# Performance work log

Hardware: AMD Instinct MI355X
Metric: run time of the kernel (lower is better)

Reference implementation:

```python
import jax, jax.numpy as jnp
import numpy as np

EMBED = 1024
HEADS = 16
HEAD_DIM = EMBED // HEADS


def setup_inputs() -> dict:
    key = jax.random.key(0)
    ks = jax.random.split(key, 11)
    B, L, D = 2, 2048, EMBED
    s = 0.02
    return {
        "q": jax.random.normal(ks[0], (B, L, D), jnp.float32),
        "k": jax.random.normal(ks[1], (B, L, D), jnp.float32),
        "v": jax.random.normal(ks[2], (B, L, D), jnp.float32),
        "w_q": jax.random.normal(ks[3], (D, D), jnp.float32) * s,
        "b_q": jnp.zeros((D,), jnp.float32),
        "w_k": jax.random.normal(ks[4], (D, D), jnp.float32) * s,
        "b_k": jnp.zeros((D,), jnp.float32),
        "w_v": jax.random.normal(ks[5], (D, D), jnp.float32) * s,
        "b_v": jnp.zeros((D,), jnp.float32),
        "w_o": jax.random.normal(ks[6], (D, D), jnp.float32) * s,
        "b_o": jnp.zeros((D,), jnp.float32),
    }


def reference(q, k, v, w_q, b_q, w_k, b_k, w_v, b_v, w_o, b_o):
    B, L, D = q.shape
    H, Dh = HEADS, HEAD_DIM
    # Linear projections (torch Linear: x @ W.T + b)
    qp = (q @ w_q.T + b_q).reshape(B, L, H, Dh)
    kp = (k @ w_k.T + b_k).reshape(B, L, H, Dh)
    vp = (v @ w_v.T + b_v).reshape(B, L, H, Dh)
    # energy: [n, h, q, k]
    energy = jnp.einsum("nqhd,nkhd->nhqk", qp, kp)
    scale = 1.0 / jnp.sqrt(jnp.asarray(Dh, qp.dtype))
    attn = jax.nn.softmax(energy * scale, axis=-1)
    ctx = jnp.einsum("nhql,nlhd->nqhd", attn, vp).reshape(B, L, D)
    return ctx @ w_o.T + b_o
```

## Files before the change

### kernel.cpp

```cpp
#include <hip/hip_runtime.h>

typedef __bf16 bf16;
typedef __bf16 bf16x2 __attribute__((ext_vector_type(2)));
typedef __bf16 bf16x4 __attribute__((ext_vector_type(4)));
typedef __bf16 bf16x8 __attribute__((ext_vector_type(8)));
typedef float f32x4 __attribute__((ext_vector_type(4)));

#define MFMA16(a, b, c) __builtin_amdgcn_mfma_f32_16x16x32_bf16((a), (b), (c), 0, 0, 0)

#define QSCALE 0.18033688011112042f

__device__ inline void gld16(const void* g, void* l) {
    __builtin_amdgcn_global_load_lds(
        (const __attribute__((address_space(1))) unsigned int*)g,
        (__attribute__((address_space(3))) unsigned int*)l, 16, 0, 0);
}

__device__ inline bf16x8 cvt8(float4 a, float4 b) {
    bf16x8 v;
    v[0] = (bf16)a.x; v[1] = (bf16)a.y; v[2] = (bf16)a.z; v[3] = (bf16)a.w;
    v[4] = (bf16)b.x; v[5] = (bf16)b.y; v[6] = (bf16)b.z; v[7] = (bf16)b.w;
    return v;
}

__global__ __launch_bounds__(256) void cvt7_kernel(
    const float* __restrict__ q,  bf16* __restrict__ qb,
    const float* __restrict__ k,  bf16* __restrict__ kb,
    const float* __restrict__ v,  bf16* __restrict__ vb,
    const float* __restrict__ wq, bf16* __restrict__ wqb,
    const float* __restrict__ wk, bf16* __restrict__ wkb,
    const float* __restrict__ wv, bf16* __restrict__ wvb,
    const float* __restrict__ wo, bf16* __restrict__ wob)
{
    const float* src; bf16* dst; int n;
    switch (blockIdx.y) {
        case 0: src = q;  dst = qb;  n = 1 << 22; break;
        case 1: src = k;  dst = kb;  n = 1 << 22; break;
        case 2: src = v;  dst = vb;  n = 1 << 22; break;
        case 3: src = wq; dst = wqb; n = 1 << 20; break;
        case 4: src = wk; dst = wkb; n = 1 << 20; break;
        case 5: src = wv; dst = wvb; n = 1 << 20; break;
        default: src = wo; dst = wob; n = 1 << 20; break;
    }
    int i = (blockIdx.x * 256 + threadIdx.x) * 8;
    if (i < n) {
        float4 a = *(const float4*)&src[i];
        float4 b = *(const float4*)&src[i + 4];
        *(bf16x8*)&dst[i] = cvt8(a, b);
    }
}

__global__ __launch_bounds__(256) void cvt3_kernel(
    const float* __restrict__ s0, bf16* __restrict__ d0,
    const float* __restrict__ s1, bf16* __restrict__ d1,
    const float* __restrict__ s2, bf16* __restrict__ d2)
{
    const float* src = blockIdx.y == 0 ? s0 : blockIdx.y == 1 ? s1 : s2;
    bf16*        dst = blockIdx.y == 0 ? d0 : blockIdx.y == 1 ? d1 : d2;
    int i = (blockIdx.x * 256 + threadIdx.x) * 8;
    float4 a = *(const float4*)&src[i];
    float4 b = *(const float4*)&src[i + 4];
    *(bf16x8*)&dst[i] = cvt8(a, b);
}

__global__ __launch_bounds__(256) void cvt_kernel(
    const float* __restrict__ src, bf16* __restrict__ dst, int n)
{
    int i = (blockIdx.x * 256 + threadIdx.x) * 8;
    if (i < n) {
        float4 a = *(const float4*)&src[i];
        float4 b = *(const float4*)&src[i + 4];
        *(bf16x8*)&dst[i] = cvt8(a, b);
    }
}

__global__ __launch_bounds__(256) void qkv_bf16(
    const bf16* __restrict__ qb, const bf16* __restrict__ kb,
    const bf16* __restrict__ vb,
    const bf16* __restrict__ wq, const float* __restrict__ bq,
    const bf16* __restrict__ wk, const float* __restrict__ bk,
    const bf16* __restrict__ wv, const float* __restrict__ bv,
    bf16* __restrict__ Qp, bf16* __restrict__ Kp, bf16* __restrict__ Vt)
{
    __shared__ __align__(16) bf16 sm[16896];
    bf16* As = sm;
    bf16* Bs = sm + 8192;
    bf16* Ts = sm;

    const int id  = blockIdx.x;
    const int pr  = (id >> 6) * 8 + (id & 7);
    const int proj = pr >> 5;
    const int m0  = (pr & 31) * 128;
    const int n0  = ((id >> 3) & 7) * 128;

    const bf16*  A    = proj == 0 ? qb : proj == 1 ? kb : vb;
    const bf16*  B    = proj == 0 ? wq : proj == 1 ? wk : wv;
    const float* bias = proj == 0 ? bq : proj == 1 ? bk : bv;

    const int tid  = threadIdx.x;
    const int lane = tid & 63;
    const int w    = tid >> 6;
    const int g    = lane >> 4;
    const int ln   = lane & 15;
    const int rowb = (w & 1) * 64;
    const int colb = (w >> 1) * 64;
    const int ro   = lane >> 3, lc = lane & 7;

    auto issue = [&](int t) {
        int k0 = t * 64;
        for (int j = 0; j < 4; ++j) {
            int base = w * 32 + j * 8;
            int row  = base + ro;
            int c    = lc ^ (row & 7);
            gld16(&A[(size_t)(m0 + row) * 1024 + k0 + c * 8], &As[base * 64]);
            gld16(&B[(size_t)(n0 + row) * 1024 + k0 + c * 8], &Bs[base * 64]);
        }
    };

    issue(0);
    f32x4 acc[4][4] = {};

    for (int t = 0; t < 16; ++t) {
        __syncthreads();
        for (int ks = 0; ks < 2; ++ks) {
            bf16x8 af[4], bfm[4];
            for (int mi = 0; mi < 4; ++mi) {
                int row = rowb + mi * 16 + ln;
                af[mi] = *(const bf16x8*)&As[row * 64 + ((ks * 4 + g) ^ (ln & 7)) * 8];
            }
            for (int ni = 0; ni < 4; ++ni) {
                int row = colb + ni * 16 + ln;
                bfm[ni] = *(const bf16x8*)&Bs[row * 64 + ((ks * 4 + g) ^ (ln & 7)) * 8];
            }
            for (int mi = 0; mi < 4; ++mi)
                for (int ni = 0; ni < 4; ++ni)
                    acc[mi][ni] = MFMA16(af[mi], bfm[ni], acc[mi][ni]);
        }
        __syncthreads();
        if (t < 15) issue(t + 1);
    }

    if (proj != 2) {
        for (int mi = 0; mi < 4; ++mi) {
            for (int ni = 0; ni < 4; ++ni) {
                int col = n0 + colb + ni * 16 + ln;
                float bv_ = bias[col];
                int rowbase = m0 + rowb + mi * 16 + g * 4;
                if (proj == 0) {
                    for (int r = 0; r < 4; ++r)
                        Qp[(size_t)(rowbase + r) * 1024 + col] =
                            (bf16)((acc[mi][ni][r] + bv_) * QSCALE);
                } else {
                    for (int r = 0; r < 4; ++r)
                        Kp[(size_t)(rowbase + r) * 1024 + col] =
                            (bf16)(acc[mi][ni][r] + bv_);
                }
            }
        }
    } else {
        for (int mi = 0; mi < 4; ++mi) {
            for (int ni = 0; ni < 4; ++ni) {
                int col = colb + ni * 16 + ln;
                float bv_ = bias[n0 + col];
                int row = rowb + mi * 16 + g * 4;
                bf16x4 pk;
                for (int r = 0; r < 4; ++r) pk[r] = (bf16)(acc[mi][ni][r] + bv_);
                *(bf16x4*)&Ts[col * 132 + row] = pk;
            }
        }
        __syncthreads();
        const int bidx = m0 >> 11;
        const int tok0 = m0 & 2047;
        for (int i = 0; i < 8; ++i) {
            int c    = tid + 256 * i;
            int col  = c >> 4;
            int t64  = (c >> 3) & 1;
            int cc   = c & 7;
            int gcol = n0 + col;
            union { bf16 e[8]; uint4 u; } tmp;
            for (int j = 0; j < 8; ++j) {
                int s = 2 * cc + (j >> 2) + ((j & 3) << 4);
                tmp.e[j] = Ts[col * 132 + t64 * 64 + s];
            }
            size_t dst = ((size_t)(bidx * 16 + (gcol >> 6)) * 64 + (gcol & 63)) * 2048
                         + tok0 + t64 * 64 + cc * 8;
            *(uint4*)&Vt[dst] = tmp.u;
        }
    }
}

__global__ __launch_bounds__(256) void qkv_gemm(
    const float* __restrict__ q, const float* __restrict__ k,
    const float* __restrict__ v,
    const bf16* __restrict__ wq, const float* __restrict__ bq,
    const bf16* __restrict__ wk, const float* __restrict__ bk,
    const bf16* __restrict__ wv, const float* __restrict__ bv,
    bf16* __restrict__ Qp, bf16* __restrict__ Kp, bf16* __restrict__ Vt)
{
    __shared__ __align__(16) bf16 sm[8192 + 2 * 8192];
    bf16* As = sm;
    bf16* Bs = sm + 8192;
    bf16* Ts = sm;

    const int id  = blockIdx.x;
    const int pr  = (id >> 6) * 8 + (id & 7);
    const int proj = pr >> 5;
    const int m0  = (pr & 31) * 128;
    const int n0  = ((id >> 3) & 7) * 128;

    const float* A    = proj == 0 ? q  : proj == 1 ? k  : v;
    const bf16*  B    = proj == 0 ? wq : proj == 1 ? wk : wv;
    const float* bias = proj == 0 ? bq : proj == 1 ? bk : bv;

    const int tid  = threadIdx.x;
    const int lane = tid & 63;
    const int w    = tid >> 6;
    const int g    = lane >> 4;
    const int ln   = lane & 15;
    const int rowb = (w & 1) * 64;
    const int colb = (w >> 1) * 64;
    const int srow = tid >> 3, slc = tid & 7;
    const int ro   = lane >> 3, lc = lane & 7;

    float4 ra[4][2];
    for (int i = 0; i < 4; ++i) {
        const float* p = &A[(size_t)(m0 + srow + 32 * i) * 1024 + slc * 8];
        ra[i][0] = *(const float4*)p;
        ra[i][1] = *(const float4*)(p + 4);
    }
    for (int j = 0; j < 4; ++j) {
        int base = w * 32 + j * 8;
        int row  = base + ro;
        int c    = lc ^ (row & 7);
        gld16(&B[(size_t)(n0 + row) * 1024 + c * 8], &Bs[base * 64]);
    }

    f32x4 acc[4][4] = {};

    for (int t = 0; t < 16; ++t) {
        __syncthreads();
        for (int i = 0; i < 4; ++i) {
            int row = srow + 32 * i;
            *(bf16x8*)&As[row * 64 + (slc ^ (row & 7)) * 8] = cvt8(ra[i][0], ra[i][1]);
        }
        __syncthreads();
        if (t < 15) {
            int k1 = (t + 1) * 64;
            for (int i = 0; i < 4; ++i) {
                const float* p = &A[(size_t)(m0 + srow + 32 * i) * 1024 + k1 + slc * 8];
                ra[i][0] = *(const float4*)p;
                ra[i][1] = *(const float4*)(p + 4);
            }
            int bsel = (t + 1) & 1;
            for (int j = 0; j < 4; ++j) {
                int base = w * 32 + j * 8;
                int row  = base + ro;
                int c    = lc ^ (row & 7);
                gld16(&B[(size_t)(n0 + row) * 1024 + k1 + c * 8],
                      &Bs[bsel * 8192 + base * 64]);
            }
        }
        const bf16* Bt = Bs + (t & 1) * 8192;
        for (int ks = 0; ks < 2; ++ks) {
            bf16x8 af[4], bfm[4];
            for (int mi = 0; mi < 4; ++mi) {
                int row = rowb + mi * 16 + ln;
                af[mi] = *(const bf16x8*)&As[row * 64 + ((ks * 4 + g) ^ (ln & 7)) * 8];
            }
            for (int ni = 0; ni < 4; ++ni) {
                int row = colb + ni * 16 + ln;
                bfm[ni] = *(const bf16x8*)&Bt[row * 64 + ((ks * 4 + g) ^ (ln & 7)) * 8];
            }
            for (int mi = 0; mi < 4; ++mi)
                for (int ni = 0; ni < 4; ++ni)
                    acc[mi][ni] = MFMA16(af[mi], bfm[ni], acc[mi][ni]);
        }
    }

    if (proj != 2) {
        for (int mi = 0; mi < 4; ++mi) {
            for (int ni = 0; ni < 4; ++ni) {
                int col = n0 + colb + ni * 16 + ln;
                float bv_ = bias[col];
                int rowbase = m0 + rowb + mi * 16 + g * 4;
                if (proj == 0) {
                    for (int r = 0; r < 4; ++r)
                        Qp[(size_t)(rowbase + r) * 1024 + col] =
                            (bf16)((acc[mi][ni][r] + bv_) * QSCALE);
                } else {
                    for (int r = 0; r < 4; ++r)
                        Kp[(size_t)(rowbase + r) * 1024 + col] =
                            (bf16)(acc[mi][ni][r] + bv_);
                }
            }
        }
    } else {
        __syncthreads();
        for (int mi = 0; mi < 4; ++mi) {
            for (int ni = 0; ni < 4; ++ni) {
                int col = colb + ni * 16 + ln;
                float bv_ = bias[n0 + col];
                int row = rowb + mi * 16 + g * 4;
                bf16x4 pk;
                for (int r = 0; r < 4; ++r) pk[r] = (bf16)(acc[mi][ni][r] + bv_);
                *(bf16x4*)&Ts[col * 132 + row] = pk;
            }
        }
        __syncthreads();
        const int bidx = m0 >> 11;
        const int tok0 = m0 & 2047;
        for (int i = 0; i < 8; ++i) {
            int c    = tid + 256 * i;
            int col  = c >> 4;
            int t64  = (c >> 3) & 1;
            int cc   = c & 7;
            int gcol = n0 + col;
            union { bf16 e[8]; uint4 u; } tmp;
            for (int j = 0; j < 8; ++j) {
                int s = 2 * cc + (j >> 2) + ((j & 3) << 4);
                tmp.e[j] = Ts[col * 132 + t64 * 64 + s];
            }
            size_t dst = ((size_t)(bidx * 16 + (gcol >> 6)) * 64 + (gcol & 63)) * 2048
                         + tok0 + t64 * 64 + cc * 8;
            *(uint4*)&Vt[dst] = tmp.u;
        }
    }
}

__global__ __launch_bounds__(256) void gemm_out(
    const bf16* __restrict__ A, const bf16* __restrict__ B,
    const float* __restrict__ bias, float* __restrict__ C)
{
    __shared__ __align__(16) bf16 sm[2 * 4096 + 2 * 8192];
    bf16* As = sm;
    bf16* Bs = sm + 8192;

    const int id = blockIdx.x;
    const int m0 = ((id >> 6) * 8 + (id & 7)) * 64;
    const int n0 = ((id >> 3) & 7) * 128;

    const int tid  = threadIdx.x;
    const int lane = tid & 63;
    const int w    = tid >> 6;
    const int g    = lane >> 4;
    const int ln   = lane & 15;
    const int rowb = (w & 1) * 32;
    const int colb = (w >> 1) * 64;
    const int ro   = lane >> 3, lc = lane & 7;

    auto issue = [&](int t) {
        int k0 = t * 64, sel = t & 1;
        for (int j = 0; j < 2; ++j) {
            int base = w * 16 + j * 8;
            int row  = base + ro;
            int c    = lc ^ (row & 7);
            gld16(&A[(size_t)(m0 + row) * 1024 + k0 + c * 8],
                  &As[sel * 4096 + base * 64]);
        }
        for (int j = 0; j < 4; ++j) {
            int base = w * 32 + j * 8;
            int row  = base + ro;
            int c    = lc ^ (row & 7);
            gld16(&B[(size_t)(n0 + row) * 1024 + k0 + c * 8],
                  &Bs[sel * 8192 + base * 64]);
        }
    };

    issue(0);
    f32x4 acc[2][4] = {};

    for (int t = 0; t < 16; ++t) {
        __syncthreads();
        if (t < 15) issue(t + 1);
        const bf16* At = As + (t & 1) * 4096;
        const bf16* Bt = Bs + (t & 1) * 8192;
        for (int ks = 0; ks < 2; ++ks) {
            bf16x8 af[2], bfm[4];
            for (int mi = 0; mi < 2; ++mi) {
                int row = rowb + mi * 16 + ln;
                af[mi] = *(const bf16x8*)&At[row * 64 + ((ks * 4 + g) ^ (ln & 7)) * 8];
            }
            for (int ni = 0; ni < 4; ++ni) {
                int row = colb + ni * 16 + ln;
                bfm[ni] = *(const bf16x8*)&Bt[row * 64 + ((ks * 4 + g) ^ (ln & 7)) * 8];
            }
            for (int mi = 0; mi < 2; ++mi)
                for (int ni = 0; ni < 4; ++ni)
                    acc[mi][ni] = MFMA16(af[mi], bfm[ni], acc[mi][ni]);
        }
    }

    for (int mi = 0; mi < 2; ++mi) {
        for (int ni = 0; ni < 4; ++ni) {
            int col = n0 + colb + ni * 16 + ln;
            float bv_ = bias[col];
            int rowbase = m0 + rowb + mi * 16 + g * 4;
            for (int r = 0; r < 4; ++r)
                C[(size_t)(rowbase + r) * 1024 + col] = acc[mi][ni][r] + bv_;
        }
    }
}

__global__ __launch_bounds__(256, 2) void attn_kernel(
    const bf16* __restrict__ Qp, const bf16* __restrict__ Kp,
    const bf16* __restrict__ Vt, bf16* __restrict__ Ctx)
{
    __shared__ __align__(16) bf16 smem[2 * 4096 + 2 * 4096];
    bf16* Ks = smem;
    bf16* Vs = smem + 8192;

    const int id = blockIdx.x;
    const int qt = (id >> 3) & 15;
    const int bh = (id & 7) + ((id >> 7) << 3);

    const int tid  = threadIdx.x;
    const int lane = tid & 63;
    const int w    = tid >> 6;
    const int g    = lane >> 4;
    const int ln   = lane & 15;
    const int ro   = lane >> 3, lc = lane & 7;
    const size_t rowQ0 = (size_t)(bh >> 4) * 2048 + qt * 128;
    const size_t rowK0 = (size_t)(bh >> 4) * 2048;
    const int hcol = (bh & 15) * 64;
    const bf16* VtB = Vt + (size_t)bh * 64 * 2048;

    for (int j = 0; j < 2; ++j) {
        int base = w * 16 + j * 8;
        int row  = base + ro;
        int c    = lc ^ (row & 7);
        gld16(&Kp[(rowK0 + row) * 1024 + hcol + c * 8], &Ks[base * 64]);
        gld16(&VtB[(size_t)row * 2048 + c * 8], &Vs[base * 64]);
    }

    bf16x8 qf[2][2];
#pragma unroll
    for (int u = 0; u < 2; ++u)
#pragma unroll
        for (int ks = 0; ks < 2; ++ks)
            qf[u][ks] = *(const bf16x8*)&Qp[(rowQ0 + w * 32 + u * 16 + ln) * 1024
                                            + hcol + ks * 32 + g * 8];

    bf16x8 ones;
#pragma unroll
    for (int i = 0; i < 8; ++i) ones[i] = (bf16)1.0f;

    f32x4 oacc[2][4] = {};
    f32x4 lacc[2] = {};

    __syncthreads();

    for (int t = 0; t < 32; ++t) {
        if (t < 31) {
            int sel = (t + 1) & 1, kvo = (t + 1) * 64;
            for (int j = 0; j < 2; ++j) {
                int base = w * 16 + j * 8;
                int kv   = base + ro;
                int c    = lc ^ (kv & 7);
                gld16(&Kp[(rowK0 + kvo + kv) * 1024 + hcol + c * 8],
                      &Ks[sel * 4096 + base * 64]);
                gld16(&VtB[(size_t)kv * 2048 + kvo + c * 8],
                      &Vs[sel * 4096 + base * 64]);
            }
        }
        const bf16* Kt  = Ks + (t & 1) * 4096;
        const bf16* Vti = Vs + (t & 1) * 4096;

        f32x4 sf[2][4] = {};
#pragma unroll
        for (int ks = 0; ks < 2; ++ks) {
            bf16x8 kf[4];
#pragma unroll
            for (int nj = 0; nj < 4; ++nj) {
                int row = nj * 16 + ln;
                kf[nj] = *(const bf16x8*)&Kt[row * 64 + ((ks * 4 + g) ^ (ln & 7)) * 8];
            }
            __builtin_amdgcn_s_setprio(1);
#pragma unroll
            for (int u = 0; u < 2; ++u)
#pragma unroll
                for (int nj = 0; nj < 4; ++nj)
                    sf[u][nj] = MFMA16(kf[nj], qf[u][ks], sf[u][nj]);
            __builtin_amdgcn_s_setprio(0);
        }

        unsigned W[2][4][2];
#pragma unroll
        for (int u = 0; u < 2; ++u)
#pragma unroll
            for (int r = 0; r < 4; ++r)
#pragma unroll
                for (int h = 0; h < 2; ++h) {
                    bf16x2 t2;
                    t2[0] = (bf16)__builtin_amdgcn_exp2f(sf[u][2 * h][r]);
                    t2[1] = (bf16)__builtin_amdgcn_exp2f(sf[u][2 * h + 1][r]);
                    W[u][r][h] = __builtin_bit_cast(unsigned, t2);
                }
#pragma unroll
        for (int u = 0; u < 2; ++u)
#pragma unroll
            for (int h = 0; h < 2; ++h) {
                asm("v_permlane16_swap_b32 %0, %1" : "+v"(W[u][0][h]), "+v"(W[u][2][h]));
                asm("v_permlane32_swap_b32 %0, %1" : "+v"(W[u][0][h]), "+v"(W[u][2][h]));
                asm("v_permlane16_swap_b32 %0, %1" : "+v"(W[u][1][h]), "+v"(W[u][3][h]));
                asm("v_permlane32_swap_b32 %0, %1" : "+v"(W[u][1][h]), "+v"(W[u][3][h]));
            }

#pragma unroll
        for (int ks = 0; ks < 2; ++ks) {
            bf16x8 vf[4];
#pragma unroll
            for (int nd = 0; nd < 4; ++nd) {
                int row = nd * 16 + ln;
                vf[nd] = *(const bf16x8*)&Vti[row * 64 + ((ks * 4 + g) ^ (ln & 7)) * 8];
            }
            __builtin_amdgcn_s_setprio(1);
#pragma unroll
            for (int u = 0; u < 2; ++u) {
                union { unsigned uw[4]; bf16x8 v; } pf;
                pf.uw[0] = W[u][2 * ks][0];     pf.uw[1] = W[u][2 * ks][1];
                pf.uw[2] = W[u][2 * ks + 1][0]; pf.uw[3] = W[u][2 * ks + 1][1];
                lacc[u] = MFMA16(pf.v, ones, lacc[u]);
#pragma unroll
                for (int nd = 0; nd < 4; ++nd)
                    oacc[u][nd] = MFMA16(pf.v, vf[nd], oacc[u][nd]);
            }
            __builtin_amdgcn_s_setprio(0);
        }
        __syncthreads();
    }

#pragma unroll
    for (int u = 0; u < 2; ++u)
#pragma unroll
        for (int r = 0; r < 4; ++r) {
            float inv = 1.0f / lacc[u][r];
            size_t row = rowQ0 + w * 32 + u * 16 + g * 4 + r;
#pragma unroll
            for (int nd = 0; nd < 4; ++nd)
                Ctx[row * 1024 + hcol + nd * 16 + ln] = (bf16)(oacc[u][nd][r] * inv);
        }
}

extern "C" void kernel_launch(void* const* d_in, const int* in_sizes, int n_in,
                              void* d_out, int out_size, void* d_ws, size_t ws_size,
                              hipStream_t stream)
{
    const float* q  = (const float*)d_in[0];
    const float* k  = (const float*)d_in[1];
    const float* v  = (const float*)d_in[2];
    const float* wq = (const float*)d_in[3];
    const float* bq = (const float*)d_in[4];
    const float* wk = (const float*)d_in[5];
    const float* bk = (const float*)d_in[6];
    const float* wv = (const float*)d_in[7];
    const float* bv = (const float*)d_in[8];
    const float* wo = (const float*)d_in[9];
    const float* bo = (const float*)d_in[10];
    float* out = (float*)d_out;

    const int D = 1024;
    bf16* W  = (bf16*)d_ws;
    bf16* Qp = W;
    bf16* Kp = W + (1u << 22);
    bf16* Vt = W + (2u << 22);
    bf16* Ctx = Qp;

    if (ws_size >= (size_t)40 * 1024 * 1024) {
        bf16* vb  = W + (3u << 22);
        bf16* wqb = W + (1u << 24);
        bf16* wkb = wqb + (1u << 20);
        bf16* wvb = wkb + (1u << 20);
        bf16* wob = wvb + (1u << 20);
        bf16* qb  = (bf16*)d_out;
        bf16* kb  = qb + (1u << 22);

        cvt7_kernel<<<dim3(2048, 7), 256, 0, stream>>>(
            q, qb, k, kb, v, vb, wq, wqb, wk, wkb, wv, wvb, wo, wob);
        qkv_bf16<<<768, 256, 0, stream>>>(qb, kb, vb, wqb, bq, wkb, bk, wvb, bv,
                                          Qp, Kp, Vt);
        attn_kernel<<<512, 256, 0, stream>>>(Qp, Kp, Vt, Ctx);
        gemm_out<<<512, 256, 0, stream>>>(Ctx, wob, bo, out);
    } else {
        bf16* wqb = (bf16*)d_out;
        bf16* wkb = wqb + (size_t)D * D;
        bf16* wvb = wkb + (size_t)D * D;
        bf16* wob = Kp;

        cvt3_kernel<<<dim3(512, 3), 256, 0, stream>>>(wq, wqb, wk, wkb, wv, wvb);
        qkv_gemm<<<768, 256, 0, stream>>>(q, k, v, wqb, bq, wkb, bk, wvb, bv,
                                          Qp, Kp, Vt);
        attn_kernel<<<512, 256, 0, stream>>>(Qp, Kp, Vt, Ctx);
        cvt_kernel<<<512, 256, 0, stream>>>(wo, wob, D * D);
        gemm_out<<<512, 256, 0, stream>>>(Ctx, wob, bo, out);
    }
}
```

Before: 208.4 us.

## Split attention KV range across two wave groups and merge partials in LDS

The attention block grows to 512 threads: two groups of four waves each process half of the key/value sequence for the same 128 query rows, each with its own double-buffered LDS tiles. At the end, group 0 writes its unnormalized output and row sums to shared memory, and group 1 adds them to its own before normalizing and storing. This shortens the serial KV loop per wave and raises waves per CU to hide latency. It costs more LDS per block (64KB), an extra reduction step and barrier, and occupancy limits from the larger shared memory footprint. The merge needs no max rescaling because the kernel already skips the running max in its softmax.

```diff
diff --git a/kernel.cpp b/kernel.cpp
--- a/kernel.cpp
+++ b/kernel.cpp
@@ -401,13 +401,15 @@
     }
 }
 
-__global__ __launch_bounds__(256, 2) void attn_kernel(
+__global__ __launch_bounds__(512, 4) void attn_kernel(
     const bf16* __restrict__ Qp, const bf16* __restrict__ Kp,
     const bf16* __restrict__ Vt, bf16* __restrict__ Ctx)
 {
-    __shared__ __align__(16) bf16 smem[2 * 4096 + 2 * 4096];
+    __shared__ __align__(16) bf16 smem[32768];
     bf16* Ks = smem;
-    bf16* Vs = smem + 8192;
+    bf16* Vs = smem + 16384;
+    float* O_sh = (float*)smem;
+    float* l_sh = (float*)smem + 64 * 132;
 
     const int id = blockIdx.x;
     const int qt = (id >> 3) & 15;
@@ -416,20 +418,25 @@
     const int tid  = threadIdx.x;
     const int lane = tid & 63;
     const int w    = tid >> 6;
+    const int h    = w >> 2;
+    const int wl   = w & 3;
     const int g    = lane >> 4;
     const int ln   = lane & 15;
     const int ro   = lane >> 3, lc = lane & 7;
+    const int kvb  = h * 1024;
     const size_t rowQ0 = (size_t)(bh >> 4) * 2048 + qt * 128;
     const size_t rowK0 = (size_t)(bh >> 4) * 2048;
     const int hcol = (bh & 15) * 64;
     const bf16* VtB = Vt + (size_t)bh * 64 * 2048;
 
     for (int j = 0; j < 2; ++j) {
-        int base = w * 16 + j * 8;
+        int base = wl * 16 + j * 8;
         int row  = base + ro;
         int c    = lc ^ (row & 7);
-        gld16(&Kp[(rowK0 + row) * 1024 + hcol + c * 8], &Ks[base * 64]);
-        gld16(&VtB[(size_t)row * 2048 + c * 8], &Vs[base * 64]);
+        gld16(&Kp[(rowK0 + kvb + row) * 1024 + hcol + c * 8],
+              &Ks[(h * 2 + 0) * 4096 + base * 64]);
+        gld16(&VtB[(size_t)row * 2048 + kvb + c * 8],
+              &Vs[(h * 2 + 0) * 4096 + base * 64]);
     }
 
     bf16x8 qf[2][2];
@@ -437,7 +444,7 @@
     for (int u = 0; u < 2; ++u)
 #pragma unroll
         for (int ks = 0; ks < 2; ++ks)
-            qf[u][ks] = *(const bf16x8*)&Qp[(rowQ0 + w * 32 + u * 16 + ln) * 1024
+            qf[u][ks] = *(const bf16x8*)&Qp[(rowQ0 + wl * 32 + u * 16 + ln) * 1024
                                             + hcol + ks * 32 + g * 8];
 
     bf16x8 ones;
@@ -449,21 +456,21 @@
 
     __syncthreads();
 
-    for (int t = 0; t < 32; ++t) {
-        if (t < 31) {
-            int sel = (t + 1) & 1, kvo = (t + 1) * 64;
+    for (int t = 0; t < 16; ++t) {
+        if (t < 15) {
+            int sel = (t + 1) & 1, kvo = kvb + (t + 1) * 64;
             for (int j = 0; j < 2; ++j) {
-                int base = w * 16 + j * 8;
-                int kv   = base + ro;
-                int c    = lc ^ (kv & 7);
-                gld16(&Kp[(rowK0 + kvo + kv) * 1024 + hcol + c * 8],
-                      &Ks[sel * 4096 + base * 64]);
-                gld16(&VtB[(size_t)kv * 2048 + kvo + c * 8],
-                      &Vs[sel * 4096 + base * 64]);
-            }
-        }
-        const bf16* Kt  = Ks + (t & 1) * 4096;
-        const bf16* Vti = Vs + (t & 1) * 4096;
+                int base = wl * 16 + j * 8;
+                int row  = base + ro;
+                int c    = lc ^ (row & 7);
+                gld16(&Kp[(rowK0 + kvo + row) * 1024 + hcol + c * 8],
+                      &Ks[(h * 2 + sel) * 4096 + base * 64]);
+                gld16(&VtB[(size_t)row * 2048 + kvo + c * 8],
+                      &Vs[(h * 2 + sel) * 4096 + base * 64]);
+            }
+        }
+        const bf16* Kt  = Ks + (h * 2 + (t & 1)) * 4096;
+        const bf16* Vti = Vs + (h * 2 + (t & 1)) * 4096;
 
         f32x4 sf[2][4] = {};
 #pragma unroll
@@ -489,20 +496,20 @@
 #pragma unroll
             for (int r = 0; r < 4; ++r)
 #pragma unroll
-                for (int h = 0; h < 2; ++h) {
+                for (int hh = 0; hh < 2; ++hh) {
                     bf16x2 t2;
-                    t2[0] = (bf16)__builtin_amdgcn_exp2f(sf[u][2 * h][r]);
-                    t2[1] = (bf16)__builtin_amdgcn_exp2f(sf[u][2 * h + 1][r]);
-                    W[u][r][h] = __builtin_bit_cast(unsigned, t2);
+                    t2[0] = (bf16)__builtin_amdgcn_exp2f(sf[u][2 * hh][r]);
+                    t2[1] = (bf16)__builtin_amdgcn_exp2f(sf[u][2 * hh + 1][r]);
+                    W[u][r][hh] = __builtin_bit_cast(unsigned, t2);
                 }
 #pragma unroll
         for (int u = 0; u < 2; ++u)
 #pragma unroll
-            for (int h = 0; h < 2; ++h) {
-                asm("v_permlane16_swap_b32 %0, %1" : "+v"(W[u][0][h]), "+v"(W[u][2][h]));
-                asm("v_permlane32_swap_b32 %0, %1" : "+v"(W[u][0][h]), "+v"(W[u][2][h]));
-                asm("v_permlane16_swap_b32 %0, %1" : "+v"(W[u][1][h]), "+v"(W[u][3][h]));
-                asm("v_permlane32_swap_b32 %0, %1" : "+v"(W[u][1][h]), "+v"(W[u][3][h]));
+            for (int hh = 0; hh < 2; ++hh) {
+                asm("v_permlane16_swap_b32 %0, %1" : "+v"(W[u][0][hh]), "+v"(W[u][2][hh]));
+                asm("v_permlane32_swap_b32 %0, %1" : "+v"(W[u][0][hh]), "+v"(W[u][2][hh]));
+                asm("v_permlane16_swap_b32 %0, %1" : "+v"(W[u][1][hh]), "+v"(W[u][3][hh]));
+                asm("v_permlane32_swap_b32 %0, %1" : "+v"(W[u][1][hh]), "+v"(W[u][3][hh]));
             }
 
 #pragma unroll
@@ -529,16 +536,38 @@
         __syncthreads();
     }
 
-#pragma unroll
-    for (int u = 0; u < 2; ++u)
-#pragma unroll
-        for (int r = 0; r < 4; ++r) {
-            float inv = 1.0f / lacc[u][r];
-            size_t row = rowQ0 + w * 32 + u * 16 + g * 4 + r;
+    if (h == 0) {
+#pragma unroll
+        for (int u = 0; u < 2; ++u) {
 #pragma unroll
             for (int nd = 0; nd < 4; ++nd)
-                Ctx[row * 1024 + hcol + nd * 16 + ln] = (bf16)(oacc[u][nd][r] * inv);
-        }
+                *(f32x4*)&O_sh[(nd * 16 + ln) * 132 + wl * 32 + u * 16 + g * 4] =
+                    oacc[u][nd];
+            if (ln == 0)
+                *(f32x4*)&l_sh[wl * 32 + u * 16 + g * 4] = lacc[u];
+        }
+    }
+    __syncthreads();
+    if (h == 1) {
+#pragma unroll
+        for (int u = 0; u < 2; ++u) {
+            f32x4 l4 = *(const f32x4*)&l_sh[wl * 32 + u * 16 + g * 4];
+            f32x4 inv;
+#pragma unroll
+            for (int r = 0; r < 4; ++r) inv[r] = 1.0f / (lacc[u][r] + l4[r]);
+#pragma unroll
+            for (int nd = 0; nd < 4; ++nd) {
+                f32x4 o4 = *(const f32x4*)&O_sh[(nd * 16 + ln) * 132
+                                                + wl * 32 + u * 16 + g * 4];
+#pragma unroll
+                for (int r = 0; r < 4; ++r) {
+                    size_t row = rowQ0 + wl * 32 + u * 16 + g * 4 + r;
+                    Ctx[row * 1024 + hcol + nd * 16 + ln] =
+                        (bf16)((oacc[u][nd][r] + o4[r]) * inv[r]);
+                }
+            }
+        }
+    }
 }
 
 extern "C" void kernel_launch(void* const* d_in, const int* in_sizes, int n_in,
@@ -578,7 +607,7 @@
             q, qb, k, kb, v, vb, wq, wqb, wk, wkb, wv, wvb, wo, wob);
         qkv_bf16<<<768, 256, 0, stream>>>(qb, kb, vb, wqb, bq, wkb, bk, wvb, bv,
                                           Qp, Kp, Vt);
-        attn_kernel<<<512, 256, 0, stream>>>(Qp, Kp, Vt, Ctx);
+        attn_kernel<<<512, 512, 0, stream>>>(Qp, Kp, Vt, Ctx);
         gemm_out<<<512, 256, 0, stream>>>(Ctx, wob, bo, out);
     } else {
         bf16* wqb = (bf16*)d_out;
@@ -589,7 +618,7 @@
         cvt3_kernel<<<dim3(512, 3), 256, 0, stream>>>(wq, wqb, wk, wkb, wv, wvb);
         qkv_gemm<<<768, 256, 0, stream>>>(q, k, v, wqb, bq, wkb, bk, wvb, bv,
                                           Qp, Kp, Vt);
-        attn_kernel<<<512, 256, 0, stream>>>(Qp, Kp, Vt, Ctx);
+        attn_kernel<<<512, 512, 0, stream>>>(Qp, Kp, Vt, Ctx);
         cvt_kernel<<<512, 256, 0, stream>>>(wo, wob, D * D);
         gemm_out<<<512, 256, 0, stream>>>(Ctx, wob, bo, out);
     }
```

Result: faster. 195.2 us (-6.3%).
